# Kernel optimization log

Measured on AMD Instinct MI355X. Metric: run time of the kernel, lower is better.

## Reference

```python
import jax, jax.numpy as jnp
import numpy as np

B, L, D = 4, 2048, 1024
H, DK, DV = 16, 64, 64


def setup_inputs() -> dict:
    key = jax.random.key(0)
    ks = jax.random.split(key, 11)
    s = 1.0 / np.sqrt(D)
    so = 1.0 / np.sqrt(H * DV)
    return {
        "query": jax.random.normal(ks[0], (B, L, D), jnp.float32),
        "key": jax.random.normal(ks[1], (B, L, D), jnp.float32),
        "value": jax.random.normal(ks[2], (B, L, D), jnp.float32),
        "W_q": jax.random.uniform(ks[3], (D, H * DK), jnp.float32, -s, s),
        "b_q": jax.random.uniform(ks[4], (H * DK,), jnp.float32, -s, s),
        "W_k": jax.random.uniform(ks[5], (D, H * DK), jnp.float32, -s, s),
        "b_k": jax.random.uniform(ks[6], (H * DK,), jnp.float32, -s, s),
        "W_v": jax.random.uniform(ks[7], (D, H * DV), jnp.float32, -s, s),
        "b_v": jax.random.uniform(ks[8], (H * DV,), jnp.float32, -s, s),
        "W_o": jax.random.uniform(ks[9], (H * DV, D), jnp.float32, -so, so),
        "b_o": jax.random.uniform(ks[10], (D,), jnp.float32, -so, so),
    }


def reference(query, key, value, W_q, b_q, W_k, b_k, W_v, b_v, W_o, b_o):
    # QKV projections, then split heads: [B, L, H*d] -> [B, H, L, d]
    q = (query @ W_q + b_q).reshape(B, L, H, DK).transpose(0, 2, 1, 3)
    k = (key @ W_k + b_k).reshape(B, L, H, DK).transpose(0, 2, 1, 3)
    v = (value @ W_v + b_v).reshape(B, L, H, DV).transpose(0, 2, 1, 3)
    # scaled dot-product attention: softmax(q k^T / sqrt(dk)) v
    scores = jnp.einsum("bhqd,bhkd->bhqk", q, k) / jnp.sqrt(jnp.float32(DK))
    attn = jax.nn.softmax(scores, axis=-1)
    ctx = jnp.einsum("bhqk,bhkd->bhqd", attn, v)
    # combine heads: [B, H, L, dv] -> [B, L, H*dv], output projection
    out = ctx.transpose(0, 2, 1, 3).reshape(B, L, H * DV) @ W_o + b_o
    return out
```

## Files before the change

### kernel.cpp

```cpp
#include <hip/hip_runtime.h>

#define BATCH 4
#define LSEQ 2048
#define DMODEL 1024
#define NHEAD 16
#define DHEAD 64
#define MTOT (BATCH * LSEQ)

typedef _Float16 f16;
typedef _Float16 f16x8 __attribute__((ext_vector_type(8)));
typedef _Float16 f16x4 __attribute__((ext_vector_type(4)));
typedef float f32x4 __attribute__((ext_vector_type(4)));

#define SCORE_SCALE 0.180336878f

typedef const __attribute__((address_space(1))) void gvoid;
typedef __attribute__((address_space(3))) void lvoid;
#define GLDS16(g, l) __builtin_amdgcn_global_load_lds((gvoid*)(g), (lvoid*)(l), 16, 0, 0)

__global__ __launch_bounds__(256)
void cvt3_f32_f16(const float* __restrict__ in0, const float* __restrict__ in1,
                  const float* __restrict__ in2, f16* __restrict__ out, int n8)
{
    const int y = blockIdx.y;
    const float* in = (y == 0) ? in0 : (y == 1) ? in1 : in2;
    f16* o = out + (size_t)y * (size_t)n8 * 8;
    int i = blockIdx.x * 256 + threadIdx.x;
    if (i >= n8) return;
    float4 a = ((const float4*)in)[2 * i];
    float4 b = ((const float4*)in)[2 * i + 1];
    f16x8 v;
    v[0] = (f16)a.x; v[1] = (f16)a.y; v[2] = (f16)a.z; v[3] = (f16)a.w;
    v[4] = (f16)b.x; v[5] = (f16)b.y; v[6] = (f16)b.z; v[7] = (f16)b.w;
    ((f16x8*)o)[i] = v;
}

__global__ __launch_bounds__(256)
void wconv4(const float* __restrict__ W0, const float* __restrict__ W1,
            const float* __restrict__ W2, const float* __restrict__ W3,
            f16* __restrict__ WtBase)
{
    __shared__ float T[64][68];
    const int z = blockIdx.z;
    const float* W = (z == 0) ? W0 : (z == 1) ? W1 : (z == 2) ? W2 : W3;
    f16* Wt = WtBase + (size_t)z * DMODEL * DMODEL;
    const int t = threadIdx.x;
    const int k0 = blockIdx.y * 64, n0 = blockIdx.x * 64;
    const int tr = t >> 4, tc = (t & 15) * 4;
#pragma unroll
    for (int p = 0; p < 64; p += 16) {
        float4 v = *(const float4*)&W[(size_t)(k0 + tr + p) * DMODEL + n0 + tc];
        *(float4*)&T[tr + p][tc] = v;
    }
    __syncthreads();
    const int n = t >> 2, kc = (t & 3) * 16;
    f16x8 o0, o1;
#pragma unroll
    for (int j = 0; j < 8; ++j) o0[j] = (f16)T[kc + j][n];
#pragma unroll
    for (int j = 0; j < 8; ++j) o1[j] = (f16)T[kc + 8 + j][n];
    *(f16x8*)&Wt[(size_t)(n0 + n) * DMODEL + k0 + kc] = o0;
    *(f16x8*)&Wt[(size_t)(n0 + n) * DMODEL + k0 + kc + 8] = o1;
}

__global__ __launch_bounds__(256)
void gemm_f16(const f16* __restrict__ A, const f16* __restrict__ Bt,
              const float* __restrict__ b0, const float* __restrict__ b1,
              const float* __restrict__ b2, void* __restrict__ Cout, int fused)
{
    __shared__ f16 As[128][32];
    __shared__ f16 Bs[128][32];

    const int t = threadIdx.x;
    const int lane = t & 63, w = t >> 6;
    const int quad = lane >> 4, m16 = lane & 15;
    const int n0 = blockIdx.x * 128;
    const int m0 = blockIdx.y * 128;
    const int wm = (w & 1) * 64, wn = (w >> 1) * 64;

    const int which = fused ? (n0 >> 10) : 0;

    f32x4 acc[4][4] = {};

    const f16* Ag = A + (size_t)which * MTOT * DMODEL
                      + (size_t)(m0 + (t >> 2)) * DMODEL + (t & 3) * 8;
    const f16* Bg = Bt + (size_t)(n0 + (t >> 2)) * DMODEL + (t & 3) * 8;
    f16* Al = &As[0][0] + t * 8;
    f16* Bl = &Bs[0][0] + t * 8;

    for (int k0 = 0; k0 < DMODEL; k0 += 32) {
        __syncthreads();
        GLDS16(Ag + k0, Al);
        GLDS16(Ag + k0 + (size_t)64 * DMODEL, Al + 2048);
        GLDS16(Bg + k0, Bl);
        GLDS16(Bg + k0 + (size_t)64 * DMODEL, Bl + 2048);
        __syncthreads();
        f16x8 af[4], bf[4];
#pragma unroll
        for (int mi = 0; mi < 4; ++mi)
            af[mi] = *(const f16x8*)&As[wm + mi * 16 + m16][quad * 8];
#pragma unroll
        for (int ni = 0; ni < 4; ++ni)
            bf[ni] = *(const f16x8*)&Bs[wn + ni * 16 + m16][quad * 8];
#pragma unroll
        for (int mi = 0; mi < 4; ++mi)
#pragma unroll
            for (int ni = 0; ni < 4; ++ni)
                acc[mi][ni] = __builtin_amdgcn_mfma_f32_16x16x32_f16(
                    af[mi], bf[ni], acc[mi][ni], 0, 0, 0);
    }

    if (fused) {
        const float* bp = (which == 0) ? b0 : (which == 1) ? b1 : b2;
        const float scale = (which == 0) ? SCORE_SCALE : 1.0f;
        f16* o = (f16*)Cout + (size_t)which * MTOT * DMODEL;
#pragma unroll
        for (int ni = 0; ni < 4; ++ni) {
            const int nn = (n0 + wn + ni * 16 + m16) & 1023;
            const float bv = bp[nn];
            const int h = nn >> 6, d = nn & 63;
#pragma unroll
            for (int mi = 0; mi < 4; ++mi) {
#pragma unroll
                for (int j = 0; j < 4; ++j) {
                    const int m = m0 + wm + mi * 16 + quad * 4 + j;
                    const int b = m >> 11, l = m & (LSEQ - 1);
                    const float v = (acc[mi][ni][j] + bv) * scale;
                    if (which < 2)
                        o[(((size_t)(b * NHEAD + h) * LSEQ + l) << 6) + d] = (f16)v;
                    else
                        o[(((size_t)(b * NHEAD + h) << 6) + d) * LSEQ + l] = (f16)v;
                }
            }
        }
    } else {
#pragma unroll
        for (int ni = 0; ni < 4; ++ni) {
            const int n = n0 + wn + ni * 16 + m16;
            const float bv = b0[n];
#pragma unroll
            for (int mi = 0; mi < 4; ++mi)
#pragma unroll
                for (int j = 0; j < 4; ++j) {
                    const int m = m0 + wm + mi * 16 + quad * 4 + j;
                    ((float*)Cout)[(size_t)m * DMODEL + n] = acc[mi][ni][j] + bv;
                }
        }
    }
}

__global__ __launch_bounds__(256, 2)
void attn_mfma(const f16* __restrict__ Qh, const f16* __restrict__ Kh,
               const f16* __restrict__ Vt, f16* __restrict__ ctx)
{
    __shared__ f16 Ks[2][64][32];
    __shared__ f16 Vs[2][64][32];
    __shared__ f16 Ps[256][72];

    const int t = threadIdx.x;
    const int lane = t & 63, w = t >> 6;
    const int quad = lane >> 4, m16 = lane & 15;

    const int bid = blockIdx.x;
    const int x = bid & 7, rest = bid >> 3;
    const int qt = rest & 7;
    const int g = x + 8 * (rest >> 3);
    const int q0 = qt * 256, wq = w * 64;

    const f16* Qg = Qh + (size_t)g * LSEQ * DHEAD;
    const f16* Kg = Kh + (size_t)g * LSEQ * DHEAD;
    const f16* Vg = Vt + (size_t)g * LSEQ * DHEAD;

    f16x8 qa[4][2];
#pragma unroll
    for (int qi = 0; qi < 4; ++qi)
#pragma unroll
        for (int ks = 0; ks < 2; ++ks)
            qa[qi][ks] = *(const f16x8*)&Qg[(size_t)(q0 + wq + qi * 16 + m16) * DHEAD
                                            + ks * 32 + quad * 8];

    f32x4 ctxa[4][4] = {};
    float lsum[4] = {0.f, 0.f, 0.f, 0.f};

    const f16* ksrc = Kg + (size_t)(t >> 2) * DHEAD + (t & 3) * 8;
    const f16* vsrc = Vg + (size_t)(t >> 2) * LSEQ + (t & 3) * 8;
    f16* kdst = &Ks[0][0][0] + t * 8;
    f16* vdst = &Vs[0][0][0] + t * 8;

    for (int kt = 0; kt < LSEQ; kt += 64) {
        __syncthreads();
        GLDS16(ksrc + (size_t)kt * DHEAD, kdst);
        GLDS16(ksrc + (size_t)kt * DHEAD + 32, kdst + 2048);
        GLDS16(vsrc + kt, vdst);
        GLDS16(vsrc + kt + 32, vdst + 2048);
        __syncthreads();

        f16x8 kb[4][2];
#pragma unroll
        for (int ki = 0; ki < 4; ++ki)
#pragma unroll
            for (int ks = 0; ks < 2; ++ks)
                kb[ki][ks] = *(const f16x8*)&Ks[ks][ki * 16 + m16][quad * 8];

        f32x4 s[4][4];
#pragma unroll
        for (int ki = 0; ki < 4; ++ki)
#pragma unroll
            for (int qi = 0; qi < 4; ++qi) {
                f32x4 z = {0.f, 0.f, 0.f, 0.f};
                z = __builtin_amdgcn_mfma_f32_16x16x32_f16(kb[ki][0], qa[qi][0], z, 0, 0, 0);
                s[ki][qi] = __builtin_amdgcn_mfma_f32_16x16x32_f16(kb[ki][1], qa[qi][1], z, 0, 0, 0);
            }

#pragma unroll
        for (int ki = 0; ki < 4; ++ki)
#pragma unroll
            for (int qi = 0; qi < 4; ++qi) {
                f16x4 pk;
#pragma unroll
                for (int j = 0; j < 4; ++j) {
                    const float p = __builtin_amdgcn_exp2f(s[ki][qi][j]);
                    lsum[qi] += p;
                    pk[j] = (f16)p;
                }
                *(f16x4*)&Ps[wq + qi * 16 + m16][ki * 16 + quad * 4] = pk;
            }

        f16x8 pa[4][2], vb[4][2];
#pragma unroll
        for (int qi = 0; qi < 4; ++qi)
#pragma unroll
            for (int ks = 0; ks < 2; ++ks)
                pa[qi][ks] = *(const f16x8*)&Ps[wq + qi * 16 + m16][ks * 32 + quad * 8];
#pragma unroll
        for (int di = 0; di < 4; ++di)
#pragma unroll
            for (int ks = 0; ks < 2; ++ks)
                vb[di][ks] = *(const f16x8*)&Vs[ks][di * 16 + m16][quad * 8];
#pragma unroll
        for (int qi = 0; qi < 4; ++qi)
#pragma unroll
            for (int di = 0; di < 4; ++di) {
                ctxa[qi][di] = __builtin_amdgcn_mfma_f32_16x16x32_f16(pa[qi][0], vb[di][0], ctxa[qi][di], 0, 0, 0);
                ctxa[qi][di] = __builtin_amdgcn_mfma_f32_16x16x32_f16(pa[qi][1], vb[di][1], ctxa[qi][di], 0, 0, 0);
            }
    }

    float linv[4];
#pragma unroll
    for (int qi = 0; qi < 4; ++qi) {
        float l = lsum[qi];
        l += __shfl_xor(l, 16);
        l += __shfl_xor(l, 32);
        linv[qi] = 1.0f / l;
    }

    const int batch = g >> 4, h = g & 15;
#pragma unroll
    for (int qi = 0; qi < 4; ++qi)
#pragma unroll
        for (int j = 0; j < 4; ++j) {
            const float inv = __shfl(linv[qi], quad * 4 + j);
            const int l = q0 + wq + qi * 16 + quad * 4 + j;
#pragma unroll
            for (int di = 0; di < 4; ++di) {
                const int col = h * 64 + di * 16 + m16;
                ctx[((size_t)batch * LSEQ + l) * DMODEL + col] = (f16)(ctxa[qi][di][j] * inv);
            }
        }
}

extern "C" void kernel_launch(void* const* d_in, const int* in_sizes, int n_in,
                              void* d_out, int out_size, void* d_ws, size_t ws_size,
                              hipStream_t stream)
{
    const float* query = (const float*)d_in[0];
    const float* key   = (const float*)d_in[1];
    const float* value = (const float*)d_in[2];
    const float* W_q   = (const float*)d_in[3];
    const float* b_q   = (const float*)d_in[4];
    const float* W_k   = (const float*)d_in[5];
    const float* b_k   = (const float*)d_in[6];
    const float* W_v   = (const float*)d_in[7];
    const float* b_v   = (const float*)d_in[8];
    const float* W_o   = (const float*)d_in[9];
    const float* b_o   = (const float*)d_in[10];
    float* out = (float*)d_out;

    const size_t MAT = (size_t)MTOT * DMODEL;
    f16* base = (f16*)d_ws;
    f16* Aq   = base;
    f16* Qhp  = base + 3 * MAT;
    f16* ctxh = base + 6 * MAT;
    f16* Wtq  = base + 7 * MAT;
    f16* Wto  = Wtq + (size_t)3 * DMODEL * DMODEL;

    const int n8 = (int)(MAT / 8);
    cvt3_f32_f16<<<dim3(n8 / 256, 3), 256, 0, stream>>>(query, key, value, Aq, n8);
    wconv4<<<dim3(DMODEL / 64, DMODEL / 64, 4), 256, 0, stream>>>(W_q, W_k, W_v, W_o, Wtq);

    gemm_f16<<<dim3(3 * DMODEL / 128, MTOT / 128), 256, 0, stream>>>(
        Aq, Wtq, b_q, b_k, b_v, Qhp, 1);

    attn_mfma<<<BATCH * NHEAD * (LSEQ / 256), 256, 0, stream>>>(
        Qhp, Qhp + MAT, Qhp + 2 * MAT, ctxh);

    gemm_f16<<<dim3(DMODEL / 128, MTOT / 128), 256, 0, stream>>>(
        ctxh, Wto, b_o, nullptr, nullptr, out, 0);
}
```

Measured before the change: 373.8 us.

## Deepen GEMM K-step to 64, swap grid order, vectorize V-transposed stores

```diff
diff --git a/kernel.cpp b/kernel.cpp
--- a/kernel.cpp
+++ b/kernel.cpp
@@ -68,14 +68,14 @@
               const float* __restrict__ b0, const float* __restrict__ b1,
               const float* __restrict__ b2, void* __restrict__ Cout, int fused)
 {
-    __shared__ f16 As[128][32];
-    __shared__ f16 Bs[128][32];
+    __shared__ f16 As2[2][128][32];
+    __shared__ f16 Bs2[2][128][32];
 
     const int t = threadIdx.x;
     const int lane = t & 63, w = t >> 6;
     const int quad = lane >> 4, m16 = lane & 15;
-    const int n0 = blockIdx.x * 128;
-    const int m0 = blockIdx.y * 128;
+    const int m0 = blockIdx.x * 128;
+    const int n0 = blockIdx.y * 128;
     const int wm = (w & 1) * 64, wn = (w >> 1) * 64;
 
     const int which = fused ? (n0 >> 10) : 0;
@@ -85,29 +85,35 @@
     const f16* Ag = A + (size_t)which * MTOT * DMODEL
                       + (size_t)(m0 + (t >> 2)) * DMODEL + (t & 3) * 8;
     const f16* Bg = Bt + (size_t)(n0 + (t >> 2)) * DMODEL + (t & 3) * 8;
-    f16* Al = &As[0][0] + t * 8;
-    f16* Bl = &Bs[0][0] + t * 8;
-
-    for (int k0 = 0; k0 < DMODEL; k0 += 32) {
+    f16* Al = &As2[0][0][0] + t * 8;
+    f16* Bl = &Bs2[0][0][0] + t * 8;
+
+    for (int k0 = 0; k0 < DMODEL; k0 += 64) {
         __syncthreads();
-        GLDS16(Ag + k0, Al);
-        GLDS16(Ag + k0 + (size_t)64 * DMODEL, Al + 2048);
-        GLDS16(Bg + k0, Bl);
-        GLDS16(Bg + k0 + (size_t)64 * DMODEL, Bl + 2048);
+#pragma unroll
+        for (int h = 0; h < 2; ++h) {
+            GLDS16(Ag + k0 + h * 32, Al + h * 4096);
+            GLDS16(Ag + k0 + h * 32 + (size_t)64 * DMODEL, Al + h * 4096 + 2048);
+            GLDS16(Bg + k0 + h * 32, Bl + h * 4096);
+            GLDS16(Bg + k0 + h * 32 + (size_t)64 * DMODEL, Bl + h * 4096 + 2048);
+        }
         __syncthreads();
-        f16x8 af[4], bf[4];
-#pragma unroll
-        for (int mi = 0; mi < 4; ++mi)
-            af[mi] = *(const f16x8*)&As[wm + mi * 16 + m16][quad * 8];
-#pragma unroll
-        for (int ni = 0; ni < 4; ++ni)
-            bf[ni] = *(const f16x8*)&Bs[wn + ni * 16 + m16][quad * 8];
-#pragma unroll
-        for (int mi = 0; mi < 4; ++mi)
+#pragma unroll
+        for (int h = 0; h < 2; ++h) {
+            f16x8 af[4], bf[4];
+#pragma unroll
+            for (int mi = 0; mi < 4; ++mi)
+                af[mi] = *(const f16x8*)&As2[h][wm + mi * 16 + m16][quad * 8];
 #pragma unroll
             for (int ni = 0; ni < 4; ++ni)
-                acc[mi][ni] = __builtin_amdgcn_mfma_f32_16x16x32_f16(
-                    af[mi], bf[ni], acc[mi][ni], 0, 0, 0);
+                bf[ni] = *(const f16x8*)&Bs2[h][wn + ni * 16 + m16][quad * 8];
+#pragma unroll
+            for (int mi = 0; mi < 4; ++mi)
+#pragma unroll
+                for (int ni = 0; ni < 4; ++ni)
+                    acc[mi][ni] = __builtin_amdgcn_mfma_f32_16x16x32_f16(
+                        af[mi], bf[ni], acc[mi][ni], 0, 0, 0);
+        }
     }
 
     if (fused) {
@@ -121,15 +127,19 @@
             const int h = nn >> 6, d = nn & 63;
 #pragma unroll
             for (int mi = 0; mi < 4; ++mi) {
-#pragma unroll
-                for (int j = 0; j < 4; ++j) {
-                    const int m = m0 + wm + mi * 16 + quad * 4 + j;
-                    const int b = m >> 11, l = m & (LSEQ - 1);
-                    const float v = (acc[mi][ni][j] + bv) * scale;
-                    if (which < 2)
-                        o[(((size_t)(b * NHEAD + h) * LSEQ + l) << 6) + d] = (f16)v;
-                    else
-                        o[(((size_t)(b * NHEAD + h) << 6) + d) * LSEQ + l] = (f16)v;
+                const int mrow = m0 + wm + mi * 16 + quad * 4;
+                const int b = mrow >> 11, l0 = mrow & (LSEQ - 1);
+                if (which < 2) {
+#pragma unroll
+                    for (int j = 0; j < 4; ++j) {
+                        const float v = (acc[mi][ni][j] + bv) * scale;
+                        o[(((size_t)(b * NHEAD + h) * LSEQ + l0 + j) << 6) + d] = (f16)v;
+                    }
+                } else {
+                    f16x4 pk;
+#pragma unroll
+                    for (int j = 0; j < 4; ++j) pk[j] = (f16)(acc[mi][ni][j] + bv);
+                    *(f16x4*)&o[(((size_t)(b * NHEAD + h) << 6) + d) * LSEQ + l0] = pk;
                 }
             }
         }
@@ -299,12 +309,12 @@
     cvt3_f32_f16<<<dim3(n8 / 256, 3), 256, 0, stream>>>(query, key, value, Aq, n8);
     wconv4<<<dim3(DMODEL / 64, DMODEL / 64, 4), 256, 0, stream>>>(W_q, W_k, W_v, W_o, Wtq);
 
-    gemm_f16<<<dim3(3 * DMODEL / 128, MTOT / 128), 256, 0, stream>>>(
+    gemm_f16<<<dim3(MTOT / 128, 3 * DMODEL / 128), 256, 0, stream>>>(
         Aq, Wtq, b_q, b_k, b_v, Qhp, 1);
 
     attn_mfma<<<BATCH * NHEAD * (LSEQ / 256), 256, 0, stream>>>(
         Qhp, Qhp + MAT, Qhp + 2 * MAT, ctxh);
 
-    gemm_f16<<<dim3(DMODEL / 128, MTOT / 128), 256, 0, stream>>>(
+    gemm_f16<<<dim3(MTOT / 128, DMODEL / 128), 256, 0, stream>>>(
         ctxh, Wto, b_o, nullptr, nullptr, out, 0);
 }
```

After: 332.6 us. 1.12x faster.
